# Kernel optimization log

Hardware: AMD Instinct MI355X
Metric: run time of the kernel (lower is better)

## Reference

```python
import jax, jax.numpy as jnp
from jax import lax
import numpy as np

BN_EPS = 1e-3

def _hard_sigmoid(x):
    # Keras hard_sigmoid: relu6(x + 3) / 6
    return jnp.clip(x / 6.0 + 0.5, 0.0, 1.0)

def _conv(x, w):
    # x: [B,H,W,C], w: [kh,kw,C,Cout]
    return lax.conv_general_dilated(x, w, window_strides=(1, 1), padding='SAME',
                                    dimension_numbers=('NHWC', 'HWIO', 'NHWC'))

def _convlstm(x, Wx, Wh, b):
    # x: [B,T,H,W,C] -> [B,T,H,W,F]; gates packed i,f,c,o along last dim (Keras order)
    B, T, H, W, C = x.shape
    F = b.shape[0] // 4
    h0 = jnp.zeros((B, H, W, F), x.dtype)
    c0 = jnp.zeros_like(h0)

    def step(carry, xt):
        h, c = carry
        z = _conv(xt, Wx) + _conv(h, Wh) + b  # [B,H,W,4F]
        i, f, g, o = jnp.split(z, 4, axis=-1)
        c = _hard_sigmoid(f) * c + _hard_sigmoid(i) * jnp.tanh(g)
        h = _hard_sigmoid(o) * jnp.tanh(c)
        return (h, c), h

    _, hs = lax.scan(step, (h0, c0), jnp.moveaxis(x, 1, 0))  # [T,B,H,W,F]
    return jnp.moveaxis(hs, 0, 1)


def setup_inputs() -> dict:
    key = jax.random.key(0)
    ks = jax.random.split(key, 8)
    B, T, H, W, C, F = 4, 16, 64, 64, 48, 48
    x = jax.random.normal(ks[0], (B, T, H, W, C), jnp.float32)
    s = 0.05  # keep gate pre-activations in a sane range
    Wx1 = jax.random.normal(ks[1], (3, 3, C, 4 * F), jnp.float32) * s
    Wh1 = jax.random.normal(ks[2], (3, 3, F, 4 * F), jnp.float32) * s
    b1 = jax.random.normal(ks[3], (4 * F,), jnp.float32) * s
    Wx2 = jax.random.normal(ks[4], (3, 3, F, 4 * F), jnp.float32) * s
    Wh2 = jax.random.normal(ks[5], (3, 3, F, 4 * F), jnp.float32) * s
    b2 = jax.random.normal(ks[6], (4 * F,), jnp.float32) * s
    gamma = jnp.ones((F,), jnp.float32)
    beta = jnp.zeros((F,), jnp.float32)
    mean = jax.random.normal(ks[7], (F,), jnp.float32) * 0.1
    var = jax.random.uniform(jax.random.fold_in(key, 99), (F,), jnp.float32, 0.5, 1.5)
    return {"x": x, "Wx1": Wx1, "Wh1": Wh1, "b1": b1,
            "Wx2": Wx2, "Wh2": Wh2, "b2": b2,
            "gamma": gamma, "beta": beta, "mean": mean, "var": var}


def reference(x, Wx1, Wh1, b1, Wx2, Wh2, b2, gamma, beta, mean, var):
    h = _convlstm(x, Wx1, Wh1, b1)
    # Dropout(0.2) at inference: identity. BatchNorm (inference, per-channel):
    h = gamma * (h - mean) * lax.rsqrt(var + BN_EPS) + beta
    h = _convlstm(h, Wx2, Wh2, b2)
    return x + h  # channels match (C == filters) -> direct residual add
```

## Files before the change

### kernel.cpp

```cpp
#include <hip/hip_runtime.h>
#include <hip/hip_bf16.h>

typedef __bf16 bf16;
typedef __bf16 bf16x8 __attribute__((ext_vector_type(8)));
typedef float  f32x4  __attribute__((ext_vector_type(4)));
typedef unsigned short u16x8 __attribute__((ext_vector_type(8)));

#define NB 4
#define NT 16
#define NH 64
#define NW 64
#define NC 48
#define RSTR 104
#define RKY  (66*RSTR)

__device__ __forceinline__ float hsig(float x){
    return fminf(fmaxf(x*0.16666667f + 0.5f, 0.0f), 1.0f);
}
__device__ __forceinline__ float ftanh(float x){
    float ax = fabsf(x);
    float e  = __expf(-2.0f*ax);
    float r  = (1.0f - e) * __builtin_amdgcn_rcpf(1.0f + e);
    return __builtin_copysignf(r, x);
}

__global__ void detect_dtype(const unsigned* __restrict__ g, int* __restrict__ flag){
    if (threadIdx.x == 0 && blockIdx.x == 0)
        *flag = (g[0] == 0x3F803F80u) ? 1 : 0;
}

__device__ __forceinline__ float ld_any(const void* p, int i, int isbf){
    return isbf ? (float)((const bf16*)p)[i] : ((const float*)p)[i];
}

__global__ void prep_weights(const void* __restrict__ Wx, const void* __restrict__ Wh,
                             const int* __restrict__ flag, bf16* __restrict__ Wsw){
    int isbf = *flag;
    int idx = blockIdx.x*256 + threadIdx.x;
    if (idx >= 165888) return;
    int e    = idx & 7;
    int lane = (idx >> 3) & 63;
    int nt   = (idx >> 9) % 12;
    int krk  = idx / (512*12);
    int ky = krk / 9, kr = krk % 9;
    int ln = lane & 15, lg = lane >> 4;
    int n_new  = nt*16 + ln;
    int gate = n_new & 3, c = n_new >> 2;
    int n_orig = gate*48 + c;
    int k  = kr*32 + lg*8 + e;
    int kx = k / 96, ch = k % 96;
    float v = (ch < 48) ? ld_any(Wx, ((ky*3+kx)*48 + ch)*192 + n_orig, isbf)
                        : ld_any(Wh, ((ky*3+kx)*48 + (ch-48))*192 + n_orig, isbf);
    Wsw[idx] = (bf16)v;
}

__global__ void prep_params(const void* b1, const void* b2, const void* gamma,
                            const void* beta, const void* mean, const void* var,
                            const int* __restrict__ flag, float* __restrict__ P){
    int isbf = *flag;
    int i = blockIdx.x*64 + threadIdx.x;
    if (i < 192)      P[i] = ld_any(b1, i, isbf);
    else if (i < 384) P[i] = ld_any(b2, i-192, isbf);
    else if (i < 432){
        int c = i-384;
        P[i] = ld_any(gamma,c,isbf) * rsqrtf(ld_any(var,c,isbf) + 1e-3f);
    } else if (i < 480){
        int c = i-432;
        float sc = ld_any(gamma,c,isbf) * rsqrtf(ld_any(var,c,isbf) + 1e-3f);
        P[i] = ld_any(beta,c,isbf) - ld_any(mean,c,isbf)*sc;
    }
}

__global__ __launch_bounds__(512, 1)
void fused_kernel(const void* __restrict__ x,
                  bf16* __restrict__ seq,
                  bf16* __restrict__ hA,
                  bf16* __restrict__ hB,
                  const bf16* __restrict__ Wc1,
                  const bf16* __restrict__ Wc2,
                  const float* __restrict__ P,
                  void* __restrict__ outp,
                  const int* __restrict__ flag,
                  int* __restrict__ done)
{
    __shared__ bf16  rowpad[3*RKY];
    __shared__ float zbuf[64*196];
    const int isbf = *flag;
    const int tid  = threadIdx.x;
    const int xcd  = blockIdx.x & 7;
    const int slot = blockIdx.x >> 3;
    const int img  = xcd >> 1;
    const int y    = ((xcd & 1) << 5) | slot;
    const int lane = tid & 63;
    const int wv   = tid >> 6;
    const int wn   = wv & 3;
    const int wg   = wv >> 2;
    const int ln   = lane & 15;
    const int lg   = lane >> 4;

    int* dme  = done + img*NH + y;
    int* dimg = done + img*NH;

    if (tid < 78){
        int ky = tid/26; int rmd = tid%26;
        int col = (rmd < 13) ? 0 : 65; int q = rmd % 13;
        u16x8 z = {};
        *(u16x8*)(rowpad + ky*RKY + col*RSTR + q*8) = z;
    }

    float creg[6];

    #pragma unroll
    for (int L = 0; L < 2; ++L){
        const bf16*  Wsw = L ? Wc2 : Wc1;
        const float* Pb  = P + (L ? 192 : 0);
        const void*  xs  = L ? (const void*)seq : x;
        const int    xbf = L ? 1 : isbf;

        float bi_[3], bf_[3], bg_[3], bo_[3], bns[3], bnb[3];
        #pragma unroll
        for (int q = 0; q < 3; ++q){
            int cq = (tid + q*32) % 48;
            bi_[q] = Pb[cq];      bf_[q] = Pb[48+cq];
            bg_[q] = Pb[96+cq];   bo_[q] = Pb[144+cq];
            bns[q] = P[384+cq];   bnb[q] = P[432+cq];
        }

        auto stage_x = [&](int tt){
            for (int task = tid; task < 1152; task += 512){
                int ky = task/384, chn = task%384;
                int xcol = chn/6, c0 = (chn%6)*8;
                int row = y + ky - 1;
                u16x8 val = {};
                if (row >= 0 && row < NH){
                    int si = (((img*NT + tt)*NH + row)*NW + xcol)*NC + c0;
                    if (xbf){
                        val = *(const u16x8*)((const bf16*)xs + si);
                    } else {
                        const float* src = (const float*)xs + si;
                        float4 f0 = *(const float4*)(src);
                        float4 f1 = *(const float4*)(src + 4);
                        bf16x8 v;
                        v[0]=(bf16)f0.x; v[1]=(bf16)f0.y; v[2]=(bf16)f0.z; v[3]=(bf16)f0.w;
                        v[4]=(bf16)f1.x; v[5]=(bf16)f1.y; v[6]=(bf16)f1.z; v[7]=(bf16)f1.w;
                        val = *(u16x8*)&v;
                    }
                }
                *(u16x8*)(rowpad + ky*RKY + (xcol+1)*RSTR + c0) = val;
            }
        };

        f32x4 acc[2][3];
        auto zero_acc = [&]{
            #pragma unroll
            for (int mt = 0; mt < 2; ++mt)
                #pragma unroll
                for (int j = 0; j < 3; ++j)
                    acc[mt][j] = (f32x4){0.f,0.f,0.f,0.f};
        };
        auto mfma_iter = [&](int ky, int kr){
            const bf16* wp = Wsw + (size_t)((ky*9 + kr)*12 + wn*3)*512 + lane*8;
            bf16x8 b0 = *(const bf16x8*)(wp);
            bf16x8 b1 = *(const bf16x8*)(wp + 512);
            bf16x8 b2 = *(const bf16x8*)(wp + 1024);
            const bf16* ap = rowpad + ky*RKY + (ln + (kr/3) + wg*32)*RSTR
                           + (kr%3)*32 + lg*8;
            #pragma unroll
            for (int mt = 0; mt < 2; ++mt){
                bf16x8 a = *(const bf16x8*)(ap + mt*16*RSTR);
                acc[mt][0] = __builtin_amdgcn_mfma_f32_16x16x32_bf16(a, b0, acc[mt][0], 0,0,0);
                acc[mt][1] = __builtin_amdgcn_mfma_f32_16x16x32_bf16(a, b1, acc[mt][1], 0,0,0);
                acc[mt][2] = __builtin_amdgcn_mfma_f32_16x16x32_bf16(a, b2, acc[mt][2], 0,0,0);
            }
        };
        auto groupA = [&]{
            #pragma unroll
            for (int kr = 0; kr < 9; ++kr) mfma_iter(1, kr);
            #pragma unroll
            for (int kx = 0; kx < 3; ++kx){ mfma_iter(0, kx*3); mfma_iter(2, kx*3); }
        };
        auto groupB = [&]{
            #pragma unroll
            for (int kx = 0; kx < 3; ++kx){
                mfma_iter(0, kx*3+1); mfma_iter(0, kx*3+2);
                mfma_iter(2, kx*3+1); mfma_iter(2, kx*3+2);
            }
        };

        stage_x(0);
        for (int task = tid; task < 1152; task += 512){
            int ky = task/384, chn = task%384;
            int xcol = chn/6, c0 = (chn%6)*8;
            u16x8 z = {};
            *(u16x8*)(rowpad + ky*RKY + (xcol+1)*RSTR + 48 + c0) = z;
        }
        #pragma unroll
        for (int i = 0; i < 6; ++i) creg[i] = 0.f;
        __syncthreads();

        zero_acc();
        groupA(); groupB();

        #pragma unroll 1
        for (int t = 0; t < NT; ++t){
            bf16* hw = ((t + L) & 1) ? hB : hA;

            #pragma unroll
            for (int mt = 0; mt < 2; ++mt)
                #pragma unroll
                for (int j = 0; j < 3; ++j)
                    #pragma unroll
                    for (int r = 0; r < 4; ++r)
                        zbuf[(wg*32 + mt*16 + lg*4 + r)*196 + wn*48 + j*16 + ln]
                            = acc[mt][j][r];
            __syncthreads();

            if (t < NT-1) stage_x(t+1);

            #pragma unroll
            for (int it = 0; it < 6; ++it){
                const int q = it % 3;
                int cell = tid + it*512;
                int pos = cell/48;
                int c = cell - pos*48;
                f32x4 z = *(const f32x4*)(zbuf + pos*196 + c*4);
                float cn = hsig(z[1]+bf_[q])*creg[it] + hsig(z[0]+bi_[q])*ftanh(z[2]+bg_[q]);
                float hn = hsig(z[3]+bo_[q])*ftanh(cn);
                creg[it] = cn;
                if (t < NT-1){
                    int gi = ((img*NH + y)*NW + pos)*NC + c;
                    hw[gi] = (bf16)hn;
                }
                rowpad[RKY + (pos+1)*RSTR + 48 + c] = (bf16)hn;
                int sidx = (((img*NT + t)*NH + y)*NW + pos)*NC + c;
                if (L == 0){
                    seq[sidx] = (bf16)(hn*bns[q] + bnb[q]);
                } else {
                    float xr = isbf ? (float)((const bf16*)x)[sidx]
                                    : ((const float*)x)[sidx];
                    float v = xr + hn;
                    if (isbf) ((bf16*)outp)[sidx] = (bf16)v;
                    else      ((float*)outp)[sidx] = v;
                }
            }

            __syncthreads();
            if (tid == 0)
                __hip_atomic_store(dme, L*16 + t + 1,
                                   __ATOMIC_RELEASE, __HIP_MEMORY_SCOPE_AGENT);

            if (t < NT-1){
                zero_acc();
                groupA();

                if (tid < 2){
                    int nb = tid ? y+1 : y-1;
                    if (nb >= 0 && nb < NH){
                        const int need = L*16 + t + 1;
                        while (__hip_atomic_load(dimg + nb, __ATOMIC_RELAXED,
                                                 __HIP_MEMORY_SCOPE_AGENT) < need)
                            __builtin_amdgcn_s_sleep(1);
                    }
                    __threadfence();
                }
                __syncthreads();
                for (int task = tid; task < 768; task += 512){
                    int kyh = task/384;
                    int chn = task%384;
                    int ky  = kyh << 1;
                    int xcol = chn/6, c0 = (chn%6)*8;
                    int row = y + ky - 1;
                    u16x8 val = {};
                    if (row >= 0 && row < NH)
                        val = *(const u16x8*)(hw + ((img*NH + row)*NW + xcol)*NC + c0);
                    *(u16x8*)(rowpad + ky*RKY + (xcol+1)*RSTR + 48 + c0) = val;
                }
                __syncthreads();

                groupB();
            }
        }
    }
}

extern "C" void kernel_launch(void* const* d_in, const int* in_sizes, int n_in,
                              void* d_out, int out_size, void* d_ws, size_t ws_size,
                              hipStream_t stream)
{
    const void* x     = d_in[0];
    const void* Wx1   = d_in[1];
    const void* Wh1   = d_in[2];
    const void* b1    = d_in[3];
    const void* Wx2   = d_in[4];
    const void* Wh2   = d_in[5];
    const void* b2    = d_in[6];
    const void* gamma = d_in[7];
    const void* beta  = d_in[8];
    const void* mean  = d_in[9];
    const void* var   = d_in[10];

    char* p = (char*)d_ws;
    auto carve = [&](size_t bytes)->void*{
        void* q = (void*)p; p += (bytes + 255) & ~(size_t)255; return q;
    };
    const size_t planeN = (size_t)NB*NH*NW*NC;
    int*   flag = (int*)  carve(256);
    float* P    = (float*)carve(480*sizeof(float));
    bf16*  Wc1  = (bf16*) carve(165888*sizeof(bf16));
    bf16*  Wc2  = (bf16*) carve(165888*sizeof(bf16));
    bf16*  hA   = (bf16*) carve(planeN*sizeof(bf16));
    bf16*  hB   = (bf16*) carve(planeN*sizeof(bf16));
    bf16*  seq  = (bf16*) carve((size_t)NB*NT*NH*NW*NC*sizeof(bf16));
    int*   done = (int*)  carve(NB*NH*sizeof(int));

    detect_dtype<<<1, 64, 0, stream>>>((const unsigned*)gamma, flag);
    prep_weights<<<648, 256, 0, stream>>>(Wx1, Wh1, flag, Wc1);
    prep_weights<<<648, 256, 0, stream>>>(Wx2, Wh2, flag, Wc2);
    prep_params<<<8, 64, 0, stream>>>(b1, b2, gamma, beta, mean, var, flag, P);
    hipMemsetAsync(done, 0, NB*NH*sizeof(int), stream);

    fused_kernel<<<dim3(NB*NH), dim3(512), 0, stream>>>(
        x, seq, hA, hB, Wc1, Wc2, P, d_out, flag, done);
}
```

Measured before the change: 638.1 us.

## Split conv reduction across wave groups and keep weights register-resident

The 3x3 conv reduction is split by K between two wave groups, each writing partial sums to its own LDS buffer. Group 0 computes the terms that need no neighbour rows; group 1 waits on the neighbour-row flags, loads the halo, then does the rest. Each wave now covers all 64 positions, and weights are preloaded into registers once per layer instead of reloaded every iteration. Gate biases and BN params move to LDS. The large register array together with launch_bounds(512,2) risks spills, and the dependent work after the neighbour wait is not clearly shorter than before.

```diff
diff --git a/kernel.cpp b/kernel.cpp
--- a/kernel.cpp
+++ b/kernel.cpp
@@ -71,7 +71,26 @@
     }
 }
 
-__global__ __launch_bounds__(512, 1)
+#define MF(a,b,c) __builtin_amdgcn_mfma_f32_16x16x32_bf16(a,b,c,0,0,0)
+#define KI(i, ky, kr) do{ \
+    const bf16* ap_ = rowpad + (ky)*RKY + (ln + ((kr)/3))*RSTR + ((kr)%3)*32 + lg*8; \
+    bf16x8 a0_ = *(const bf16x8*)(ap_); \
+    bf16x8 a1_ = *(const bf16x8*)(ap_ + 16*RSTR); \
+    bf16x8 a2_ = *(const bf16x8*)(ap_ + 32*RSTR); \
+    bf16x8 a3_ = *(const bf16x8*)(ap_ + 48*RSTR); \
+    acc[0][0]=MF(a0_,w[i][0],acc[0][0]); acc[0][1]=MF(a0_,w[i][1],acc[0][1]); acc[0][2]=MF(a0_,w[i][2],acc[0][2]); \
+    acc[1][0]=MF(a1_,w[i][0],acc[1][0]); acc[1][1]=MF(a1_,w[i][1],acc[1][1]); acc[1][2]=MF(a1_,w[i][2],acc[1][2]); \
+    acc[2][0]=MF(a2_,w[i][0],acc[2][0]); acc[2][1]=MF(a2_,w[i][1],acc[2][1]); acc[2][2]=MF(a2_,w[i][2],acc[2][2]); \
+    acc[3][0]=MF(a3_,w[i][0],acc[3][0]); acc[3][1]=MF(a3_,w[i][1],acc[3][1]); acc[3][2]=MF(a3_,w[i][2],acc[3][2]); \
+}while(0)
+#define WL(i, ky, kr) do{ \
+    const bf16* wp_ = Wsw + (size_t)(((ky)*9+(kr))*12 + wn*3)*512 + lane*8; \
+    w[i][0] = *(const bf16x8*)(wp_); \
+    w[i][1] = *(const bf16x8*)(wp_+512); \
+    w[i][2] = *(const bf16x8*)(wp_+1024); \
+}while(0)
+
+__global__ __launch_bounds__(512, 2)
 void fused_kernel(const void* __restrict__ x,
                   bf16* __restrict__ seq,
                   bf16* __restrict__ hA,
@@ -84,7 +103,10 @@
                   int* __restrict__ done)
 {
     __shared__ bf16  rowpad[3*RKY];
-    __shared__ float zbuf[64*196];
+    __shared__ float zbufA[64*196];
+    __shared__ float zbufB[64*196];
+    __shared__ float gbias[48*4];
+    __shared__ float bnlds[48*2];
     const int isbf = *flag;
     const int tid  = threadIdx.x;
     const int xcd  = blockIdx.x & 7;
@@ -94,7 +116,7 @@
     const int lane = tid & 63;
     const int wv   = tid >> 6;
     const int wn   = wv & 3;
-    const int wg   = wv >> 2;
+    const int kg   = wv >> 2;
     const int ln   = lane & 15;
     const int lg   = lane >> 4;
 
@@ -108,22 +130,61 @@
         *(u16x8*)(rowpad + ky*RKY + col*RSTR + q*8) = z;
     }
 
-    float creg[6];
-
-    #pragma unroll
+    float  creg[6];
+    bf16x8 w[14][3];
+    f32x4  acc[4][3];
+
+    auto acczero = [&]{
+        #pragma unroll
+        for (int mt = 0; mt < 4; ++mt)
+            #pragma unroll
+            for (int j = 0; j < 3; ++j)
+                acc[mt][j] = (f32x4){0.f,0.f,0.f,0.f};
+    };
+    auto zwrite = [&](float* zb){
+        #pragma unroll
+        for (int mt = 0; mt < 4; ++mt)
+            #pragma unroll
+            for (int j = 0; j < 3; ++j)
+                #pragma unroll
+                for (int r = 0; r < 4; ++r)
+                    zb[(mt*16 + lg*4 + r)*196 + wn*48 + j*16 + ln] = acc[mt][j][r];
+    };
+    auto mfma_kg0 = [&]{
+        KI(0,1,0);  KI(1,1,1);  KI(2,1,2);  KI(3,1,3);  KI(4,1,4);
+        KI(5,1,5);  KI(6,1,6);  KI(7,1,7);  KI(8,1,8);
+        KI(9,0,3);  KI(10,0,6); KI(11,2,0); KI(12,2,3); KI(13,2,6);
+    };
+    auto mfma_kg1 = [&]{
+        KI(0,0,0);  KI(1,0,1);  KI(2,0,2);  KI(3,0,4);  KI(4,0,5);
+        KI(5,0,7);  KI(6,0,8);  KI(7,2,1);  KI(8,2,2);  KI(9,2,4);
+        KI(10,2,5); KI(11,2,7); KI(12,2,8);
+    };
+
+    #pragma unroll 1
     for (int L = 0; L < 2; ++L){
         const bf16*  Wsw = L ? Wc2 : Wc1;
         const float* Pb  = P + (L ? 192 : 0);
         const void*  xs  = L ? (const void*)seq : x;
         const int    xbf = L ? 1 : isbf;
-
-        float bi_[3], bf_[3], bg_[3], bo_[3], bns[3], bnb[3];
-        #pragma unroll
-        for (int q = 0; q < 3; ++q){
-            int cq = (tid + q*32) % 48;
-            bi_[q] = Pb[cq];      bf_[q] = Pb[48+cq];
-            bg_[q] = Pb[96+cq];   bo_[q] = Pb[144+cq];
-            bns[q] = P[384+cq];   bnb[q] = P[432+cq];
+        const int    Loff = L*16;
+
+        if (kg == 0){
+            WL(0,1,0);  WL(1,1,1);  WL(2,1,2);  WL(3,1,3);  WL(4,1,4);
+            WL(5,1,5);  WL(6,1,6);  WL(7,1,7);  WL(8,1,8);
+            WL(9,0,3);  WL(10,0,6); WL(11,2,0); WL(12,2,3); WL(13,2,6);
+        } else {
+            WL(0,0,0);  WL(1,0,1);  WL(2,0,2);  WL(3,0,4);  WL(4,0,5);
+            WL(5,0,7);  WL(6,0,8);  WL(7,2,1);  WL(8,2,2);  WL(9,2,4);
+            WL(10,2,5); WL(11,2,7); WL(12,2,8);
+        }
+        if (tid < 48){
+            gbias[tid*4+0] = Pb[tid];
+            gbias[tid*4+1] = Pb[48+tid];
+            gbias[tid*4+2] = Pb[96+tid];
+            gbias[tid*4+3] = Pb[144+tid];
+            bnlds[tid*2+0] = P[384+tid];
+            bnlds[tid*2+1] = P[432+tid];
         }
 
         auto stage_x = [&](int tt){
@@ -150,43 +211,6 @@
             }
         };
 
-        f32x4 acc[2][3];
-        auto zero_acc = [&]{
-            #pragma unroll
-            for (int mt = 0; mt < 2; ++mt)
-                #pragma unroll
-                for (int j = 0; j < 3; ++j)
-                    acc[mt][j] = (f32x4){0.f,0.f,0.f,0.f};
-        };
-        auto mfma_iter = [&](int ky, int kr){
-            const bf16* wp = Wsw + (size_t)((ky*9 + kr)*12 + wn*3)*512 + lane*8;
-            bf16x8 b0 = *(const bf16x8*)(wp);
-            bf16x8 b1 = *(const bf16x8*)(wp + 512);
-            bf16x8 b2 = *(const bf16x8*)(wp + 1024);
-            const bf16* ap = rowpad + ky*RKY + (ln + (kr/3) + wg*32)*RSTR
-                           + (kr%3)*32 + lg*8;
-            #pragma unroll
-            for (int mt = 0; mt < 2; ++mt){
-                bf16x8 a = *(const bf16x8*)(ap + mt*16*RSTR);
-                acc[mt][0] = __builtin_amdgcn_mfma_f32_16x16x32_bf16(a, b0, acc[mt][0], 0,0,0);
-                acc[mt][1] = __builtin_amdgcn_mfma_f32_16x16x32_bf16(a, b1, acc[mt][1], 0,0,0);
-                acc[mt][2] = __builtin_amdgcn_mfma_f32_16x16x32_bf16(a, b2, acc[mt][2], 0,0,0);
-            }
-        };
-        auto groupA = [&]{
-            #pragma unroll
-            for (int kr = 0; kr < 9; ++kr) mfma_iter(1, kr);
-            #pragma unroll
-            for (int kx = 0; kx < 3; ++kx){ mfma_iter(0, kx*3); mfma_iter(2, kx*3); }
-        };
-        auto groupB = [&]{
-            #pragma unroll
-            for (int kx = 0; kx < 3; ++kx){
-                mfma_iter(0, kx*3+1); mfma_iter(0, kx*3+2);
-                mfma_iter(2, kx*3+1); mfma_iter(2, kx*3+2);
-            }
-        };
-
         stage_x(0);
         for (int task = tid; task < 1152; task += 512){
             int ky = task/384, chn = task%384;
@@ -198,34 +222,31 @@
         for (int i = 0; i < 6; ++i) creg[i] = 0.f;
         __syncthreads();
 
-        zero_acc();
-        groupA(); groupB();
+        acczero();
+        if (kg == 0){ mfma_kg0(); zwrite(zbufA); }
+        else        { mfma_kg1(); zwrite(zbufB); }
 
         #pragma unroll 1
         for (int t = 0; t < NT; ++t){
             bf16* hw = ((t + L) & 1) ? hB : hA;
-
-            #pragma unroll
-            for (int mt = 0; mt < 2; ++mt)
-                #pragma unroll
-                for (int j = 0; j < 3; ++j)
-                    #pragma unroll
-                    for (int r = 0; r < 4; ++r)
-                        zbuf[(wg*32 + mt*16 + lg*4 + r)*196 + wn*48 + j*16 + ln]
-                            = acc[mt][j][r];
             __syncthreads();
 
             if (t < NT-1) stage_x(t+1);
 
             #pragma unroll
             for (int it = 0; it < 6; ++it){
-                const int q = it % 3;
                 int cell = tid + it*512;
                 int pos = cell/48;
                 int c = cell - pos*48;
-                f32x4 z = *(const f32x4*)(zbuf + pos*196 + c*4);
-                float cn = hsig(z[1]+bf_[q])*creg[it] + hsig(z[0]+bi_[q])*ftanh(z[2]+bg_[q]);
-                float hn = hsig(z[3]+bo_[q])*ftanh(cn);
+                f32x4 zA = *(const f32x4*)(zbufA + pos*196 + c*4);
+                f32x4 zB = *(const f32x4*)(zbufB + pos*196 + c*4);
+                f32x4 gb = *(const f32x4*)(gbias + c*4);
+                float zi = zA[0]+zB[0]+gb[0];
+                float zf = zA[1]+zB[1]+gb[1];
+                float zg = zA[2]+zB[2]+gb[2];
+                float zo = zA[3]+zB[3]+gb[3];
+                float cn = hsig(zf)*creg[it] + hsig(zi)*ftanh(zg);
+                float hn = hsig(zo)*ftanh(cn);
                 creg[it] = cn;
                 if (t < NT-1){
                     int gi = ((img*NH + y)*NW + pos)*NC + c;
@@ -234,7 +255,8 @@
                 rowpad[RKY + (pos+1)*RSTR + 48 + c] = (bf16)hn;
                 int sidx = (((img*NT + t)*NH + y)*NW + pos)*NC + c;
                 if (L == 0){
-                    seq[sidx] = (bf16)(hn*bns[q] + bnb[q]);
+                    float sc = bnlds[c*2], sh = bnlds[c*2+1];
+                    seq[sidx] = (bf16)(hn*sc + sh);
                 } else {
                     float xr = isbf ? (float)((const bf16*)x)[sidx]
                                     : ((const float*)x)[sidx];
@@ -246,38 +268,45 @@
 
             __syncthreads();
             if (tid == 0)
-                __hip_atomic_store(dme, L*16 + t + 1,
+                __hip_atomic_store(dme, Loff + t + 1,
                                    __ATOMIC_RELEASE, __HIP_MEMORY_SCOPE_AGENT);
 
             if (t < NT-1){
-                zero_acc();
-                groupA();
-
-                if (tid < 2){
-                    int nb = tid ? y+1 : y-1;
-                    if (nb >= 0 && nb < NH){
-                        const int need = L*16 + t + 1;
-                        while (__hip_atomic_load(dimg + nb, __ATOMIC_RELAXED,
-                                                 __HIP_MEMORY_SCOPE_AGENT) < need)
-                            __builtin_amdgcn_s_sleep(1);
+                acczero();
+                if (kg == 0){
+                    mfma_kg0();
+                    zwrite(zbufA);
+                } else {
+                    const int need = Loff + t + 1;
+                    bool okm = (y == 0), okp = (y == NH-1);
+                    while (!(okm && okp)){
+                        if (!okm) okm = __hip_atomic_load(dimg + y-1, __ATOMIC_RELAXED,
+                                                          __HIP_MEMORY_SCOPE_AGENT) >= need;
+                        if (!okp) okp = __hip_atomic_load(dimg + y+1, __ATOMIC_RELAXED,
+                                                          __HIP_MEMORY_SCOPE_AGENT) >= need;
+                        if (!(okm && okp)) __builtin_amdgcn_s_sleep(1);
                     }
                     __threadfence();
+                    int tl = tid - 256;
+                    #pragma unroll
+                    for (int k2 = 0; k2 < 3; ++k2){
+                        int task = tl + k2*256;
+                        int kyh = task/384;
+                        int chn = task%384;
+                        int ky  = kyh << 1;
+                        int xcol = chn/6, c0 = (chn%6)*8;
+                        int row = y + ky - 1;
+                        u16x8 val = {};
+                        if (row >= 0 && row < NH)
+                            val = *(const u16x8*)(hw + ((img*NH + row)*NW + xcol)*NC + c0);
+                        *(u16x8*)(rowpad + ky*RKY + (xcol+1)*RSTR + 48 + c0) = val;
+                    }
                 }
                 __syncthreads();
-                for (int task = tid; task < 768; task += 512){
-                    int kyh = task/384;
-                    int chn = task%384;
-                    int ky  = kyh << 1;
-                    int xcol = chn/6, c0 = (chn%6)*8;
-                    int row = y + ky - 1;
-                    u16x8 val = {};
-                    if (row >= 0 && row < NH)
-                        val = *(const u16x8*)(hw + ((img*NH + row)*NW + xcol)*NC + c0);
-                    *(u16x8*)(rowpad + ky*RKY + (xcol+1)*RSTR + 48 + c0) = val;
-                }
-                __syncthreads();
-
-                groupB();
+                if (kg == 1){
+                    mfma_kg1();
+                    zwrite(zbufB);
+                }
             }
         }
     }
```

Result: slower. 1.802 ms (+182.4%).
